# Optimization experiments

Hardware: AMD Instinct MI355X
Metric: run time of the kernel (lower is better)

Reference implementation:

```python
import jax, jax.numpy as jnp
import numpy as np

N = 16384
F = 256
RATIO = 0.5
K_KEEP = int(RATIO * N)  # 8192 nodes kept


def setup_inputs() -> dict:
    key = jax.random.key(0)
    k1, k2, k3 = jax.random.split(key, 3)
    X = jax.random.normal(k1, (N, F), dtype=jnp.float32)
    # binary-ish dense adjacency
    A = (jax.random.uniform(k2, (N, N), dtype=jnp.float32) < 0.01).astype(jnp.float32)
    p = jax.random.normal(k3, (F, 1), dtype=jnp.float32)
    return {"X": X, "A": A, "p": p}


def reference(X, A, p):
    # y = X p / ||p||  (scores), shape [N, 1]
    p_hat = p / jnp.sqrt(jnp.sum(p * p))
    y = X @ p_hat
    # global top-k (single-graph mode: I == zeros), indices sorted ascending
    _, idx = jax.lax.top_k(y[:, 0], K_KEEP)
    idx = jnp.sort(idx)
    # gated features, then gather kept nodes
    features = X * jnp.tanh(y)
    X_pooled = jnp.take(features, idx, axis=0)          # [K, F]
    # adjacency submatrix A[idx, idx]
    A_pooled = jnp.take(jnp.take(A, idx, axis=0), idx, axis=1)  # [K, K]
    return X_pooled, A_pooled
```

## Files before the change

### kernel.cpp

```cpp
#include <hip/hip_runtime.h>
#include <math.h>

#define N 16384
#define F 256
#define K_KEEP 8192
#define JCH 1024
#define QS 4096

__global__ __launch_bounds__(256) void score_kernel(const float* __restrict__ X,
                                                    const float* __restrict__ p,
                                                    double* __restrict__ y,
                                                    unsigned long long* __restrict__ key) {
    const int wave = threadIdx.x >> 6;
    const int lane = threadIdx.x & 63;
    const int row  = blockIdx.x * 4 + wave;

    const float4 pv = *reinterpret_cast<const float4*>(p + lane * 4);
    const float4 xv = *reinterpret_cast<const float4*>(X + (size_t)row * F + lane * 4);

    double pp = (double)pv.x * pv.x + (double)pv.y * pv.y +
                (double)pv.z * pv.z + (double)pv.w * pv.w;
    double xp = (double)xv.x * pv.x + (double)xv.y * pv.y +
                (double)xv.z * pv.z + (double)xv.w * pv.w;

    #pragma unroll
    for (int off = 32; off >= 1; off >>= 1) {
        pp += __shfl_down(pp, off, 64);
        xp += __shfl_down(xp, off, 64);
    }
    if (lane == 0) {
        const double yy = xp / sqrt(pp);
        y[row] = yy;
        const long long b = __double_as_longlong(yy);
        key[row] = (unsigned long long)b ^
                   ((b < 0) ? 0xFFFFFFFFFFFFFFFFULL : 0x8000000000000000ULL);
    }
}

__global__ __launch_bounds__(256) void rank_kernel(const unsigned long long* __restrict__ key,
                                                   unsigned short* __restrict__ rankp) {
    __shared__ unsigned long long kch[JCH];
    const int jc    = blockIdx.y;
    const int jbase = jc * JCH;
    for (int t = threadIdx.x; t < JCH; t += 256) kch[t] = key[jbase + t];
    __syncthreads();

    const int ibase = blockIdx.x * 512 + threadIdx.x;
    const unsigned long long k0 = key[ibase];
    const unsigned long long k1 = key[ibase + 256];
    int c0 = 0, c1 = 0;
    #pragma unroll 8
    for (int jj = 0; jj < JCH; ++jj) {
        const unsigned long long kj = kch[jj];
        c0 += (int)(kj > k0);
        c1 += (int)(kj > k1);
    }
    rankp[jc * N + ibase      ] = (unsigned short)c0;
    rankp[jc * N + ibase + 256] = (unsigned short)c1;
}

__global__ __launch_bounds__(256) void flags_kernel(const unsigned short* __restrict__ rankp,
                                                    unsigned long long* __restrict__ flagbits,
                                                    int* __restrict__ blkcnt) {
    __shared__ int wc[4];
    const int b = blockIdx.x;
    const int i = b * 256 + threadIdx.x;
    int r = 0;
    #pragma unroll
    for (int jc = 0; jc < 16; ++jc) r += (int)rankp[jc * N + i];
    const bool kept = (r < K_KEEP);
    const unsigned long long m = __ballot(kept);
    const int lane = threadIdx.x & 63;
    const int wave = threadIdx.x >> 6;
    if (lane == 0) { flagbits[i >> 6] = m; wc[wave] = __popcll(m); }
    __syncthreads();
    if (threadIdx.x == 0) blkcnt[b] = wc[0] + wc[1] + wc[2] + wc[3];
}

__global__ __launch_bounds__(256) void emit_kernel(const int* __restrict__ blkcnt,
                                                   const unsigned long long* __restrict__ flagbits,
                                                   int* __restrict__ idx,
                                                   int* __restrict__ wexcl) {
    __shared__ int bc[64];
    __shared__ int woff[4];
    const int t = threadIdx.x;
    const int b = blockIdx.x;
    if (t < 64) bc[t] = blkcnt[t];
    __syncthreads();

    int goff = 0;
    for (int j = 0; j < b; ++j) goff += bc[j];

    if (t < 4) {
        int s = goff;
        for (int q = 0; q < t; ++q) s += __popcll(flagbits[4 * b + q]);
        wexcl[4 * b + t] = s;
    }

    const int i = b * 256 + t;
    const unsigned long long m = flagbits[i >> 6];
    const int lane = t & 63;
    const int wave = t >> 6;
    const bool kept = (m >> lane) & 1ull;
    if (lane == 0) woff[wave] = __popcll(m);
    __syncthreads();
    int wbase = 0;
    for (int w = 0; w < wave; ++w) wbase += woff[w];
    const int pos = __popcll(m & ((1ull << lane) - 1ull));
    if (kept) idx[goff + wbase + pos] = i;
}

__global__ __launch_bounds__(256) void xpool_kernel(const float* __restrict__ X,
                                                    const double* __restrict__ y,
                                                    const int* __restrict__ idx,
                                                    float* __restrict__ outX) {
    const int wave = threadIdx.x >> 6;
    const int lane = threadIdx.x & 63;
    const int k    = blockIdx.x * 4 + wave;
    const int src  = idx[k];
    const float tf = tanhf((float)y[src]);

    const float4 xv = *reinterpret_cast<const float4*>(X + (size_t)src * F + lane * 4);
    float4 o = {xv.x * tf, xv.y * tf, xv.z * tf, xv.w * tf};
    *reinterpret_cast<float4*>(outX + (size_t)k * F + lane * 4) = o;
}

__global__ __launch_bounds__(256) void apool_kernel(const float* __restrict__ A,
                                                    const int* __restrict__ idx,
                                                    const int* __restrict__ wexcl,
                                                    float* __restrict__ outA) {
    __shared__ float buf[QS];
    const int t   = threadIdx.x;
    const int row = blockIdx.x >> 2;
    const int h   = blockIdx.x & 3;

    const int ridx = idx[row];
    const int kb   = wexcl[h * 64];
    const int ke   = (h < 3) ? wexcl[h * 64 + 64] : K_KEEP;

    const float4* __restrict__ a4 =
        reinterpret_cast<const float4*>(A + (size_t)ridx * N + h * QS);
    float4* __restrict__ b4 = reinterpret_cast<float4*>(buf);
    #pragma unroll
    for (int s = 0; s < 4; ++s) b4[s * 256 + t] = a4[s * 256 + t];
    __syncthreads();

    float* __restrict__ orow = outA + (size_t)row * K_KEEP;
    const int qbase = h * QS;
    for (int k = kb + t; k < ke; k += 256) {
        const int src = idx[k] - qbase;
        orow[k] = buf[src];
    }
}

extern "C" void kernel_launch(void* const* d_in, const int* in_sizes, int n_in,
                              void* d_out, int out_size, void* d_ws, size_t ws_size,
                              hipStream_t stream) {
    const float* X = (const float*)d_in[0];
    const float* A = (const float*)d_in[1];
    const float* p = (const float*)d_in[2];

    float* out  = (float*)d_out;
    float* outX = out;
    float* outA = out + (size_t)K_KEEP * F;

    char* ws = (char*)d_ws;
    double*             y        = (double*)ws;
    unsigned long long* key      = (unsigned long long*)(ws + 131072);
    unsigned short*     rankp    = (unsigned short*)(ws + 262144);
    int*                idx      = (int*)(ws + 786432);
    unsigned long long* flagbits = (unsigned long long*)(ws + 819200);
    int*                blkcnt   = (int*)(ws + 821248);
    int*                wexcl    = (int*)(ws + 821504);

    score_kernel<<<N / 4, 256, 0, stream>>>(X, p, y, key);
    rank_kernel<<<dim3(32, 16), 256, 0, stream>>>(key, rankp);
    flags_kernel<<<N / 256, 256, 0, stream>>>(rankp, flagbits, blkcnt);
    emit_kernel<<<N / 256, 256, 0, stream>>>(blkcnt, flagbits, idx, wexcl);
    xpool_kernel<<<K_KEEP / 4, 256, 0, stream>>>(X, y, idx, outX);
    apool_kernel<<<K_KEEP * 4, 256, 0, stream>>>(A, idx, wexcl, outA);
}
```

Baseline: 197.1 us.

## Fuse pooling kernels, single-block emit, retile rank, vectorize gather with nontemporal IO

Changes the rank kernel to compare four keys per thread against a smaller 512-key shared chunk, giving a 16x32 grid. Compaction moves into a single-block emit kernel that prefix-sums the 256 wave masks and writes both indices and 16-bit local column offsets. The X and A pooling kernels are merged into one launch, and the A gather now writes four outputs per store using nontemporal loads and stores. The intent is to cut launch count and partial-sum overhead and to make the bandwidth-bound A gather cheaper, at the cost of a serial single-block emit step.

```diff
diff --git a/kernel.cpp b/kernel.cpp
--- a/kernel.cpp
+++ b/kernel.cpp
@@ -4,8 +4,12 @@
 #define N 16384
 #define F 256
 #define K_KEEP 8192
-#define JCH 1024
+#define JCH 512
+#define IPT 4
 #define QS 4096
+#define APOOL_BLOCKS (K_KEEP * 4)
+
+typedef float f32x4 __attribute__((ext_vector_type(4)));
 
 __global__ __launch_bounds__(256) void score_kernel(const float* __restrict__ X,
                                                     const float* __restrict__ p,
@@ -39,117 +43,120 @@
 
 __global__ __launch_bounds__(256) void rank_kernel(const unsigned long long* __restrict__ key,
                                                    unsigned short* __restrict__ rankp) {
-    __shared__ unsigned long long kch[JCH];
+    __shared__ ulonglong2 kch2[JCH / 2];
+    const int t     = threadIdx.x;
     const int jc    = blockIdx.y;
     const int jbase = jc * JCH;
-    for (int t = threadIdx.x; t < JCH; t += 256) kch[t] = key[jbase + t];
+    kch2[t] = *reinterpret_cast<const ulonglong2*>(key + jbase + 2 * t);
     __syncthreads();
 
-    const int ibase = blockIdx.x * 512 + threadIdx.x;
+    const int ibase = blockIdx.x * (256 * IPT) + t;
     const unsigned long long k0 = key[ibase];
     const unsigned long long k1 = key[ibase + 256];
-    int c0 = 0, c1 = 0;
+    const unsigned long long k2 = key[ibase + 512];
+    const unsigned long long k3 = key[ibase + 768];
+    int c0 = 0, c1 = 0, c2 = 0, c3 = 0;
     #pragma unroll 8
-    for (int jj = 0; jj < JCH; ++jj) {
-        const unsigned long long kj = kch[jj];
-        c0 += (int)(kj > k0);
-        c1 += (int)(kj > k1);
+    for (int jj = 0; jj < JCH / 2; ++jj) {
+        const ulonglong2 kk = kch2[jj];
+        c0 += (int)(kk.x > k0) + (int)(kk.y > k0);
+        c1 += (int)(kk.x > k1) + (int)(kk.y > k1);
+        c2 += (int)(kk.x > k2) + (int)(kk.y > k2);
+        c3 += (int)(kk.x > k3) + (int)(kk.y > k3);
     }
     rankp[jc * N + ibase      ] = (unsigned short)c0;
     rankp[jc * N + ibase + 256] = (unsigned short)c1;
+    rankp[jc * N + ibase + 512] = (unsigned short)c2;
+    rankp[jc * N + ibase + 768] = (unsigned short)c3;
 }
 
 __global__ __launch_bounds__(256) void flags_kernel(const unsigned short* __restrict__ rankp,
-                                                    unsigned long long* __restrict__ flagbits,
-                                                    int* __restrict__ blkcnt) {
-    __shared__ int wc[4];
-    const int b = blockIdx.x;
-    const int i = b * 256 + threadIdx.x;
+                                                    unsigned long long* __restrict__ flagbits) {
+    const int i = blockIdx.x * 256 + threadIdx.x;
     int r = 0;
     #pragma unroll
-    for (int jc = 0; jc < 16; ++jc) r += (int)rankp[jc * N + i];
+    for (int jc = 0; jc < N / JCH; ++jc) r += (int)rankp[jc * N + i];
     const bool kept = (r < K_KEEP);
     const unsigned long long m = __ballot(kept);
-    const int lane = threadIdx.x & 63;
-    const int wave = threadIdx.x >> 6;
-    if (lane == 0) { flagbits[i >> 6] = m; wc[wave] = __popcll(m); }
-    __syncthreads();
-    if (threadIdx.x == 0) blkcnt[b] = wc[0] + wc[1] + wc[2] + wc[3];
+    if ((threadIdx.x & 63) == 0) flagbits[i >> 6] = m;
 }
 
-__global__ __launch_bounds__(256) void emit_kernel(const int* __restrict__ blkcnt,
-                                                   const unsigned long long* __restrict__ flagbits,
+__global__ __launch_bounds__(256) void emit_kernel(const unsigned long long* __restrict__ flagbits,
                                                    int* __restrict__ idx,
+                                                   unsigned short* __restrict__ srcq,
                                                    int* __restrict__ wexcl) {
-    __shared__ int bc[64];
-    __shared__ int woff[4];
+    __shared__ int sc[256];
     const int t = threadIdx.x;
-    const int b = blockIdx.x;
-    if (t < 64) bc[t] = blkcnt[t];
+    const unsigned long long m = flagbits[t];
+    const int c = __popcll(m);
+    sc[t] = c;
     __syncthreads();
+    for (int off = 1; off < 256; off <<= 1) {
+        const int v = (t >= off) ? sc[t - off] : 0;
+        __syncthreads();
+        sc[t] += v;
+        __syncthreads();
+    }
+    const int excl = sc[t] - c;
+    wexcl[t] = excl;
 
-    int goff = 0;
-    for (int j = 0; j < b; ++j) goff += bc[j];
+    int base = excl;
+    unsigned long long mm = m;
+    const int col = t * 64;
+    while (mm) {
+        const int b = __ffsll((long long)mm) - 1;
+        mm &= (mm - 1);
+        const int i = col + b;
+        idx[base]  = i;
+        srcq[base] = (unsigned short)(i & (QS - 1));
+        ++base;
+    }
+}
 
-    if (t < 4) {
-        int s = goff;
-        for (int q = 0; q < t; ++q) s += __popcll(flagbits[4 * b + q]);
-        wexcl[4 * b + t] = s;
+__global__ __launch_bounds__(256) void pool_kernel(const float* __restrict__ A,
+                                                   const float* __restrict__ X,
+                                                   const double* __restrict__ y,
+                                                   const int* __restrict__ idx,
+                                                   const unsigned short* __restrict__ srcq,
+                                                   const int* __restrict__ wexcl,
+                                                   float* __restrict__ outX,
+                                                   float* __restrict__ outA) {
+    const int t = threadIdx.x;
+
+    if (blockIdx.x >= APOOL_BLOCKS) {
+        const int k    = (blockIdx.x - APOOL_BLOCKS) * 4 + (t >> 6);
+        const int lane = t & 63;
+        const int src  = idx[k];
+        const float tf = tanhf((float)y[src]);
+        const float4 xv = *reinterpret_cast<const float4*>(X + (size_t)src * F + lane * 4);
+        float4 o = {xv.x * tf, xv.y * tf, xv.z * tf, xv.w * tf};
+        *reinterpret_cast<float4*>(outX + (size_t)k * F + lane * 4) = o;
+        return;
     }
 
-    const int i = b * 256 + t;
-    const unsigned long long m = flagbits[i >> 6];
-    const int lane = t & 63;
-    const int wave = t >> 6;
-    const bool kept = (m >> lane) & 1ull;
-    if (lane == 0) woff[wave] = __popcll(m);
-    __syncthreads();
-    int wbase = 0;
-    for (int w = 0; w < wave; ++w) wbase += woff[w];
-    const int pos = __popcll(m & ((1ull << lane) - 1ull));
-    if (kept) idx[goff + wbase + pos] = i;
-}
-
-__global__ __launch_bounds__(256) void xpool_kernel(const float* __restrict__ X,
-                                                    const double* __restrict__ y,
-                                                    const int* __restrict__ idx,
-                                                    float* __restrict__ outX) {
-    const int wave = threadIdx.x >> 6;
-    const int lane = threadIdx.x & 63;
-    const int k    = blockIdx.x * 4 + wave;
-    const int src  = idx[k];
-    const float tf = tanhf((float)y[src]);
-
-    const float4 xv = *reinterpret_cast<const float4*>(X + (size_t)src * F + lane * 4);
-    float4 o = {xv.x * tf, xv.y * tf, xv.z * tf, xv.w * tf};
-    *reinterpret_cast<float4*>(outX + (size_t)k * F + lane * 4) = o;
-}
-
-__global__ __launch_bounds__(256) void apool_kernel(const float* __restrict__ A,
-                                                    const int* __restrict__ idx,
-                                                    const int* __restrict__ wexcl,
-                                                    float* __restrict__ outA) {
     __shared__ float buf[QS];
-    const int t   = threadIdx.x;
-    const int row = blockIdx.x >> 2;
-    const int h   = blockIdx.x & 3;
-
+    const int row  = blockIdx.x >> 2;
+    const int h    = blockIdx.x & 3;
     const int ridx = idx[row];
     const int kb   = wexcl[h * 64];
     const int ke   = (h < 3) ? wexcl[h * 64 + 64] : K_KEEP;
 
-    const float4* __restrict__ a4 =
-        reinterpret_cast<const float4*>(A + (size_t)ridx * N + h * QS);
-    float4* __restrict__ b4 = reinterpret_cast<float4*>(buf);
+    const f32x4* __restrict__ a4 =
+        reinterpret_cast<const f32x4*>(A + (size_t)ridx * N + h * QS);
+    f32x4* __restrict__ b4 = reinterpret_cast<f32x4*>(buf);
     #pragma unroll
-    for (int s = 0; s < 4; ++s) b4[s * 256 + t] = a4[s * 256 + t];
+    for (int s = 0; s < 4; ++s) b4[s * 256 + t] = __builtin_nontemporal_load(a4 + s * 256 + t);
     __syncthreads();
 
     float* __restrict__ orow = outA + (size_t)row * K_KEEP;
-    const int qbase = h * QS;
-    for (int k = kb + t; k < ke; k += 256) {
-        const int src = idx[k] - qbase;
-        orow[k] = buf[src];
+    const int k4b = (kb + 3) & ~3;
+    const int k4e = ke & ~3;
+    if (t < (k4b - kb)) orow[kb + t] = buf[srcq[kb + t]];
+    if (t < (ke - k4e)) orow[k4e + t] = buf[srcq[k4e + t]];
+    for (int k4 = k4b + 4 * t; k4 < k4e; k4 += 1024) {
+        const ushort4 s4 = *reinterpret_cast<const ushort4*>(srcq + k4);
+        f32x4 v = {buf[s4.x], buf[s4.y], buf[s4.z], buf[s4.w]};
+        __builtin_nontemporal_store(v, reinterpret_cast<f32x4*>(orow + k4));
     }
 }
 
@@ -168,15 +175,15 @@
     double*             y        = (double*)ws;
     unsigned long long* key      = (unsigned long long*)(ws + 131072);
     unsigned short*     rankp    = (unsigned short*)(ws + 262144);
-    int*                idx      = (int*)(ws + 786432);
-    unsigned long long* flagbits = (unsigned long long*)(ws + 819200);
-    int*                blkcnt   = (int*)(ws + 821248);
-    int*                wexcl    = (int*)(ws + 821504);
+    unsigned long long* flagbits = (unsigned long long*)(ws + 1310720);
+    int*                wexcl    = (int*)(ws + 1312768);
+    int*                idx      = (int*)(ws + 1313792);
+    unsigned short*     srcq     = (unsigned short*)(ws + 1346560);
 
     score_kernel<<<N / 4, 256, 0, stream>>>(X, p, y, key);
-    rank_kernel<<<dim3(32, 16), 256, 0, stream>>>(key, rankp);
-    flags_kernel<<<N / 256, 256, 0, stream>>>(rankp, flagbits, blkcnt);
-    emit_kernel<<<N / 256, 256, 0, stream>>>(blkcnt, flagbits, idx, wexcl);
-    xpool_kernel<<<K_KEEP / 4, 256, 0, stream>>>(X, y, idx, outX);
-    apool_kernel<<<K_KEEP * 4, 256, 0, stream>>>(A, idx, wexcl, outA);
+    rank_kernel<<<dim3(N / (256 * IPT), N / JCH), 256, 0, stream>>>(key, rankp);
+    flags_kernel<<<N / 256, 256, 0, stream>>>(rankp, flagbits);
+    emit_kernel<<<1, 256, 0, stream>>>(flagbits, idx, srcq, wexcl);
+    pool_kernel<<<APOOL_BLOCKS + K_KEEP / 4, 256, 0, stream>>>(A, X, y, idx, srcq, wexcl,
+                                                               outX, outA);
 }
```

After: 178.6 us. 1.1x faster.
